# Performance work log

Measured on AMD Instinct MI355X. Metric: run time of the kernel, lower is better.

Reference implementation:

```python
import jax, jax.numpy as jnp
import numpy as np

B, L, H, N = 8, 8192, 128, 32  # batch, seq_len, d_model, d_state//2 (complex)


def setup_inputs() -> dict:
    key = jax.random.key(0)
    ks = jax.random.split(key, 13)
    x = jax.random.normal(ks[0], (B, L, 2), dtype=jnp.float32)
    enc_w = jax.random.normal(ks[1], (2, H), dtype=jnp.float32) * (1.0 / np.sqrt(2.0))
    enc_b = jax.random.normal(ks[2], (H,), dtype=jnp.float32) * 0.01
    # S4D init: dt log-uniform in [1e-3, 1e-1], A = -0.5 + i*pi*n (S4D-Lin)
    u01 = jax.random.uniform(ks[3], (H,), dtype=jnp.float32)
    log_dt = u01 * (np.log(0.1) - np.log(0.001)) + np.log(0.001)
    log_A_real = jnp.full((H, N), np.log(0.5), dtype=jnp.float32)
    A_imag = jnp.broadcast_to(np.pi * jnp.arange(N, dtype=jnp.float32), (H, N)).copy()
    C_re = jax.random.normal(ks[4], (H, N), dtype=jnp.float32) * (0.5 ** 0.5)
    C_im = jax.random.normal(ks[5], (H, N), dtype=jnp.float32) * (0.5 ** 0.5)
    D = jax.random.normal(ks[6], (H,), dtype=jnp.float32)
    out_w = jax.random.normal(ks[7], (2 * H, H), dtype=jnp.float32) * (1.0 / np.sqrt(H))
    out_b = jax.random.normal(ks[8], (2 * H,), dtype=jnp.float32) * 0.01
    dec_w = jax.random.normal(ks[9], (H, 1), dtype=jnp.float32) * (1.0 / np.sqrt(H))
    dec_b = jax.random.normal(ks[10], (1,), dtype=jnp.float32) * 0.01
    return {"x": x, "enc_w": enc_w, "enc_b": enc_b, "log_dt": log_dt,
            "log_A_real": log_A_real, "A_imag": A_imag, "C_re": C_re,
            "C_im": C_im, "D": D, "out_w": out_w, "out_b": out_b,
            "dec_w": dec_w, "dec_b": dec_b}


def reference(x, enc_w, enc_b, log_dt, log_A_real, A_imag, C_re, C_im, D,
              out_w, out_b, dec_w, dec_b):
    # Encoder (B,L,2) -> (B,L,H), then transpose to channels-first (B,H,L)
    u = jnp.einsum('blc,ch->blh', x, enc_w) + enc_b
    u = jnp.swapaxes(u, -1, -2)  # (B,H,L)
    Lx = u.shape[-1]

    # --- S4D kernel (zero-order-hold discretization, diagonal A) ---
    dt = jnp.exp(log_dt)                      # (H,)
    A = -jnp.exp(log_A_real) + 1j * A_imag    # (H,N) complex
    C = C_re + 1j * C_im                      # (H,N)
    dtA = dt[:, None] * A                     # (H,N)
    K_coef = C * (jnp.exp(dtA) - 1.0) / A     # (H,N)
    # Vandermonde: exp(dtA * l), l = 0..L-1  -> (H,N,L)
    vand = jnp.exp(dtA[:, :, None] * jnp.arange(Lx, dtype=jnp.float32))
    K = 2.0 * jnp.einsum('hn,hnl->hl', K_coef, vand).real  # (H,L)

    # --- causal convolution via FFT (length 2L avoids circular wrap) ---
    n = 2 * Lx
    y = jnp.fft.irfft(jnp.fft.rfft(u, n) * jnp.fft.rfft(K, n), n)[..., :Lx]
    y = y + D[:, None] * u                    # skip connection

    # GELU -> pointwise GLU output projection (Conv1d(H, 2H, 1) + GLU)
    y = jax.nn.gelu(y)
    z = jnp.einsum('bhl,gh->bgl', y, out_w) + out_b[None, :, None]  # (B,2H,L)
    a, g = jnp.split(z, 2, axis=1)
    y = a * jax.nn.sigmoid(g)                 # (B,H,L)

    # Mean-pool over sequence, decode to scalar: (B,1)
    pooled = jnp.mean(y, axis=-1)             # (B,H)
    return pooled @ dec_w + dec_b
```

## Files before the change

### kernel.cpp

```cpp
#include <hip/hip_runtime.h>
#include <math.h>

#define B_ 8
#define L_ 8192
#define H_ 128
#define N_ 32
#define C_ 128
#define T_ 64


typedef _Float16 half8 __attribute__((ext_vector_type(8)));
typedef __attribute__((ext_vector_type(4))) float f32x4;

__device__ __forceinline__ float gelu_tanh(float y) {
    float t = 0.7978845608028654f * fmaf(0.044715f, y * y * y, y);
    float e = __expf(2.f * t);
    float th = 1.f - __fdividef(2.f, e + 1.f);
    return 0.5f * y * (1.f + th);
}
__device__ __forceinline__ unsigned short f2h(float f) {
    _Float16 h = (_Float16)f;
    return *(unsigned short*)&h;
}
__device__ __forceinline__ float h2f(unsigned short u) {
    return (float)(*(const _Float16*)&u);
}
__device__ __forceinline__ unsigned int pk2(float a, float b) {
    return (unsigned)f2h(a) | ((unsigned)f2h(b) << 16);
}

__global__ __launch_bounds__(256) void k_s4d(
    const float* __restrict__ x, const float* __restrict__ enc_w,
    const float* __restrict__ enc_b, const float* __restrict__ log_dt,
    const float* __restrict__ log_A_real, const float* __restrict__ A_imag,
    const float* __restrict__ C_re, const float* __restrict__ C_im,
    const float* __restrict__ Dp, const float* __restrict__ out_w,
    unsigned short* __restrict__ Wh, unsigned short* __restrict__ gy)
{
    const int bh = blockIdx.x;
    const int b = bh >> 7, h = bh & (H_ - 1);
    const int tid = threadIdx.x;
    const int lane = tid & 63, wq = tid >> 6;
    const int mrow = lane & 15, quad = lane >> 4;

    __shared__ unsigned short Ut[C_][72];
    __shared__ __align__(16) char scratch[18432];
    __shared__ float2 wTpow[7][N_];
    __shared__ float2 coefs[N_];
    __shared__ float2 ArAi[N_];
    __shared__ float  Kd[64];
    unsigned short* E16 = (unsigned short*)scratch;
    float2*         Sx  = (float2*)scratch;
    unsigned short* St  = (unsigned short*)scratch;

    const float dt = expf(log_dt[h]);
    const float Dh = Dp[h];

    if (tid < N_) {
        int n = tid;
        float Ar = -expf(log_A_real[h * N_ + n]);
        float Ai = A_imag[h * N_ + n];
        ArAi[n] = make_float2(Ar, Ai);
        float ar = dt * Ar, ai = dt * Ai;
        float er = expf(ar);
        float wr = er * cosf(ai), wi = er * sinf(ai);
        float inv = 1.f / (Ar * Ar + Ai * Ai);
        float numr = wr - 1.f, numi = wi;
        float qr = (numr * Ar + numi * Ai) * inv;
        float qi = (numi * Ar - numr * Ai) * inv;
        coefs[n] = make_float2(C_re[h * N_ + n] * qr - C_im[h * N_ + n] * qi,
                               C_re[h * N_ + n] * qi + C_im[h * N_ + n] * qr);
        float arT = dt * Ar * (float)T_, aiT = dt * Ai * (float)T_;
        float erT = expf(arT);
        float pr = erT * cosf(aiT), pi = erT * sinf(aiT);
#pragma unroll
        for (int k = 0; k < 7; ++k) {
            wTpow[k][n] = make_float2(pr, pi);
            float nr = pr * pr - pi * pi;
            pi = 2.f * pr * pi; pr = nr;
        }
    }

    if (b == 0) {
        int g = 2 * h + (tid >> 7), j = tid & 127;
        Wh[g * 128 + j] = f2h(out_w[g * 128 + j]);
    }

    const float ew0 = enc_w[h], ew1 = enc_w[H_ + h], eb = enc_b[h];
    {
        int c = tid >> 1, j0 = (tid & 1) * 32;
        const float4* xp = (const float4*)((const float2*)x + (size_t)b * L_
                                           + c * 64 + j0);
#pragma unroll
        for (int i = 0; i < 16; ++i) {
            float4 xv = xp[i];
            float u0 = fmaf(xv.x, ew0, fmaf(xv.y, ew1, eb));
            float u1 = fmaf(xv.z, ew0, fmaf(xv.w, ew1, eb));
            *(unsigned int*)&Ut[c][j0 + 2 * i] = pk2(u0, u1);
        }
    }
    __syncthreads();

    {
        int t = tid >> 2, q = tid & 3;
        float s = 0.f;
        float ft = (float)t;
#pragma unroll
        for (int k = 0; k < 8; ++k) {
            int n = q * 8 + k;
            float2 cf = coefs[n]; float2 aa = ArAi[n];
            float er = __expf(dt * aa.x * ft);
            float sn, cs; __sincosf(dt * aa.y * ft, &sn, &cs);
            s = fmaf(cf.x, er * cs, s);
            s = fmaf(-cf.y, er * sn, s);
        }
        ((float*)&Ut[t][64])[q] = s;
    }

    {
        f32x4 acc[8];
#pragma unroll
        for (int nt = 0; nt < 8; ++nt) acc[nt] = (f32x4){0.f, 0.f, 0.f, 0.f};
        const int m = wq * 16 + mrow;
        const float2 aa = ArAi[m & 31];
        const float dAr = dt * aa.x, dAi = dt * aa.y;
        const bool isIm = (m >= 32);
#pragma unroll
        for (int ks = 0; ks < 2; ++ks) {
            int k0 = ks * 32 + quad * 8;
            half8 af;
#pragma unroll
            for (int i = 0; i < 8; ++i) {
                float d = (float)(63 - (k0 + i));
                float er = __expf(dAr * d);
                float sn, cs; __sincosf(dAi * d, &sn, &cs);
                af[i] = (_Float16)(isIm ? er * sn : er * cs);
            }
#pragma unroll
            for (int nt = 0; nt < 8; ++nt) {
                half8 bf = *(const half8*)&Ut[nt * 16 + mrow][k0];
                acc[nt] = __builtin_amdgcn_mfma_f32_16x16x32_f16(
                    af, bf, acc[nt], 0, 0, 0);
            }
        }
        const int m0 = wq * 16 + quad * 4;
#pragma unroll
        for (int nt = 0; nt < 8; ++nt) {
            int cc = nt * 16 + mrow;
            unsigned long long w =
                (unsigned long long)pk2(acc[nt][0], acc[nt][1]) |
                ((unsigned long long)pk2(acc[nt][2], acc[nt][3]) << 32);
            *(unsigned long long*)&E16[cc * 72 + m0] = w;
        }
    }
    __syncthreads();

    if (tid < 64) {
        const float* kp = (const float*)&Ut[tid][64];
        Kd[tid] = 2.f * (kp[0] + kp[1] + kp[2] + kp[3])
                  + ((tid == 0) ? Dh : 0.f);
    }

    float zr[16], zi[16];
    const int cHalf = wq & 1, nHalf = wq >> 1;
    const int n0 = nHalf * 16;
    const int c = cHalf * 64 + lane;
    {
        half8 ha = *(const half8*)(E16 + c * 72 + n0);
        half8 hb = *(const half8*)(E16 + c * 72 + n0 + 8);
        half8 hc = *(const half8*)(E16 + c * 72 + 32 + n0);
        half8 hd = *(const half8*)(E16 + c * 72 + 32 + n0 + 8);
#pragma unroll
        for (int j = 0; j < 8; ++j) {
            zr[j] = (float)ha[j];  zr[8 + j] = (float)hb[j];
            zi[j] = (float)hc[j];  zi[8 + j] = (float)hd[j];
        }
    }
    __syncthreads();
#pragma unroll
    for (int k = 0; k < 6; ++k) {
        int s = 1 << k;
        float mask = (lane >= s) ? 1.f : 0.f;
#pragma unroll
        for (int j = 0; j < 16; ++j) {
            float2 q = wTpow[k][n0 + j];
            float vr = __shfl_up(zr[j], s, 64);
            float vi = __shfl_up(zi[j], s, 64);
            float adr = fmaf(q.x, vr, -(q.y * vi));
            float adi = fmaf(q.x, vi, q.y * vr);
            zr[j] = fmaf(mask, adr, zr[j]);
            zi[j] = fmaf(mask, adi, zi[j]);
        }
    }
    if (cHalf == 0) {
#pragma unroll
        for (int j = 0; j < 16; ++j)
            Sx[(n0 + j) * 64 + lane] = make_float2(zr[j], zi[j]);
    }
    __syncthreads();
    if (cHalf == 1) {
#pragma unroll
        for (int j = 0; j < 16; ++j) {
            float2 q = wTpow[6][n0 + j];
            float2 v = Sx[(n0 + j) * 64 + lane];
            zr[j] = fmaf(q.x, v.x, fmaf(-q.y, v.y, zr[j]));
            zi[j] = fmaf(q.x, v.y, fmaf(q.y, v.x, zi[j]));
        }
    }
    {
        bool l0 = (lane == 0);
#pragma unroll
        for (int j = 0; j < 16; ++j) {
            float2 bv = Sx[(n0 + j) * 64 + 63];
            float br = (cHalf == 1) ? bv.x : 0.f;
            float bi = (cHalf == 1) ? bv.y : 0.f;
            float tr = __shfl_up(zr[j], 1, 64);
            float ti = __shfl_up(zi[j], 1, 64);
            zr[j] = l0 ? br : tr;
            zi[j] = l0 ? bi : ti;
        }
    }
    __syncthreads();
    {
        uint4 w0, w1;
        w0.x = pk2(zr[0], zr[1]);   w0.y = pk2(zr[2], zr[3]);
        w0.z = pk2(zr[4], zr[5]);   w0.w = pk2(zr[6], zr[7]);
        w1.x = pk2(zr[8], zr[9]);   w1.y = pk2(zr[10], zr[11]);
        w1.z = pk2(zr[12], zr[13]); w1.w = pk2(zr[14], zr[15]);
        *(uint4*)&St[c * 72 + n0] = w0;
        *(uint4*)&St[c * 72 + n0 + 8] = w1;
        w0.x = pk2(zi[0], zi[1]);   w0.y = pk2(zi[2], zi[3]);
        w0.z = pk2(zi[4], zi[5]);   w0.w = pk2(zi[6], zi[7]);
        w1.x = pk2(zi[8], zi[9]);   w1.y = pk2(zi[10], zi[11]);
        w1.z = pk2(zi[12], zi[13]); w1.w = pk2(zi[14], zi[15]);
        *(uint4*)&St[c * 72 + 32 + n0] = w0;
        *(uint4*)&St[c * 72 + 32 + n0 + 8] = w1;
    }
    __syncthreads();

    {
        f32x4 acc[8];
#pragma unroll
        for (int nt = 0; nt < 8; ++nt) acc[nt] = (f32x4){0.f, 0.f, 0.f, 0.f};
        const int t = wq * 16 + mrow;
#pragma unroll
        for (int ks = 0; ks < 2; ++ks) {
            int k0 = ks * 32 + quad * 8;
            half8 af;
#pragma unroll
            for (int i = 0; i < 8; ++i) {
                int j = k0 + i;
                af[i] = (_Float16)((t >= j) ? Kd[t - j] : 0.f);
            }
#pragma unroll
            for (int nt = 0; nt < 8; ++nt) {
                half8 bf = *(const half8*)&Ut[nt * 16 + mrow][k0];
                acc[nt] = __builtin_amdgcn_mfma_f32_16x16x32_f16(
                    af, bf, acc[nt], 0, 0, 0);
            }
        }
        half8 afP0, afP1;
        {
            float tp1 = (float)(t + 1);
#pragma unroll
            for (int i = 0; i < 8; ++i) {
                int n = quad * 8 + i;
                float2 cf = coefs[n]; float2 aa = ArAi[n];
                float er = __expf(dt * aa.x * tp1);
                float sn, cs; __sincosf(dt * aa.y * tp1, &sn, &cs);
                float wr = er * cs, wi = er * sn;
                afP0[i] = (_Float16)( 2.f * (cf.x * wr - cf.y * wi));
                afP1[i] = (_Float16)(-2.f * (cf.x * wi + cf.y * wr));
            }
        }
#pragma unroll
        for (int ks = 0; ks < 2; ++ks) {
            int k0 = ks * 32 + quad * 8;
            half8 af = ks ? afP1 : afP0;
#pragma unroll
            for (int nt = 0; nt < 8; ++nt) {
                half8 bf = *(const half8*)&St[(nt * 16 + mrow) * 72 + k0];
                acc[nt] = __builtin_amdgcn_mfma_f32_16x16x32_f16(
                    af, bf, acc[nt], 0, 0, 0);
            }
        }
        unsigned short* gyb = gy + (size_t)bh * L_;
#pragma unroll
        for (int nt = 0; nt < 8; ++nt) {
            int cc = nt * 16 + mrow;
#pragma unroll
            for (int r = 0; r < 4; ++r) {
                int tt = wq * 16 + quad * 4 + r;
                gyb[tt * 128 + cc] = f2h(gelu_tanh(acc[nt][r]));
            }
        }
    }
}

__global__ __launch_bounds__(256) void k_mix(
    const unsigned short* __restrict__ Wh, const unsigned short* __restrict__ gy,
    const float* __restrict__ out_b, const float* __restrict__ dec_w,
    float* __restrict__ part)
{
    __shared__ unsigned short Bt[64 * 128];
    __shared__ float red[4];

    const int blk = blockIdx.x;
    const int b = blk >> 7;
    const int t = (blk >> 1) & 63, ch = blk & 1;
    const int tid = threadIdx.x;
    const int wq = tid >> 6, lane = tid & 63;

    const unsigned short* gsrc = gy + (size_t)(b * H_) * L_ + t * 128 + ch * 64;
#pragma unroll
    for (int it = 0; it < 4; ++it) {
        int idx = it * 256 + tid;
        int h = idx >> 3, v0 = (idx & 7) * 8;
        uint4 q = *(const uint4*)(gsrc + (size_t)h * L_ + v0);
        const int sw = (((h >> 3) ^ (idx & 7)) << 3) | (h & 7);
        Bt[(v0 + 0) * 128 + sw] = (unsigned short)(q.x & 0xFFFF);
        Bt[(v0 + 1) * 128 + sw] = (unsigned short)(q.x >> 16);
        Bt[(v0 + 2) * 128 + sw] = (unsigned short)(q.y & 0xFFFF);
        Bt[(v0 + 3) * 128 + sw] = (unsigned short)(q.y >> 16);
        Bt[(v0 + 4) * 128 + sw] = (unsigned short)(q.z & 0xFFFF);
        Bt[(v0 + 5) * 128 + sw] = (unsigned short)(q.z >> 16);
        Bt[(v0 + 6) * 128 + sw] = (unsigned short)(q.w & 0xFFFF);
        Bt[(v0 + 7) * 128 + sw] = (unsigned short)(q.w >> 16);
    }
    __syncthreads();

    const int ga = wq * 32;
    const int gg = 128 + wq * 32;
    const int mrow = lane & 15;
    const int quad = lane >> 4;
    f32x4 accA[2][4], accG[2][4];
#pragma unroll
    for (int mt = 0; mt < 2; ++mt)
#pragma unroll
        for (int nt = 0; nt < 4; ++nt) {
            accA[mt][nt] = (f32x4){0.f, 0.f, 0.f, 0.f};
            accG[mt][nt] = (f32x4){0.f, 0.f, 0.f, 0.f};
        }

#pragma unroll
    for (int k = 0; k < 4; ++k) {
        const int h0 = k * 32 + quad * 8;
        half8 bfr[4];
#pragma unroll
        for (int nt = 0; nt < 4; ++nt) {
            int v = nt * 16 + mrow;
            bfr[nt] = *(const half8*)&Bt[v * 128 +
                                         (((4 * k + quad) ^ (v >> 3)) << 3)];
        }
#pragma unroll
        for (int mt = 0; mt < 2; ++mt) {
            half8 ah = *(const half8*)(Wh + (ga + mt * 16 + mrow) * 128 + h0);
            half8 ag = *(const half8*)(Wh + (gg + mt * 16 + mrow) * 128 + h0);
#pragma unroll
            for (int nt = 0; nt < 4; ++nt) {
                accA[mt][nt] = __builtin_amdgcn_mfma_f32_16x16x32_f16(
                    ah, bfr[nt], accA[mt][nt], 0, 0, 0);
                accG[mt][nt] = __builtin_amdgcn_mfma_f32_16x16x32_f16(
                    ag, bfr[nt], accG[mt][nt], 0, 0, 0);
            }
        }
    }

    float s = 0.f;
#pragma unroll
    for (int mt = 0; mt < 2; ++mt) {
        float4 obA = *(const float4*)(out_b + ga + mt * 16 + quad * 4);
        float4 obG = *(const float4*)(out_b + gg + mt * 16 + quad * 4);
        float4 dv  = *(const float4*)(dec_w + ga + mt * 16 + quad * 4);
#pragma unroll
        for (int nt = 0; nt < 4; ++nt) {
#pragma unroll
            for (int r = 0; r < 4; ++r) {
                float a  = accA[mt][nt][r] + ((const float*)&obA)[r];
                float zg = accG[mt][nt][r] + ((const float*)&obG)[r];
                float sig = __fdividef(1.f, 1.f + __expf(-zg));
                s = fmaf(((const float*)&dv)[r], a * sig, s);
            }
        }
    }
#pragma unroll
    for (int off = 32; off; off >>= 1) s += __shfl_down(s, off, 64);
    if (lane == 0) red[wq] = s;
    __syncthreads();
    if (tid == 0) part[blk] = red[0] + red[1] + red[2] + red[3];
}

__global__ __launch_bounds__(512) void k_final(
    const float* __restrict__ part, const float* __restrict__ dec_b,
    float* __restrict__ out)
{
    int tid = threadIdx.x;
    int b = tid >> 6, lane = tid & 63;
    float s = part[b * 128 + lane] + part[b * 128 + 64 + lane];
#pragma unroll
    for (int off = 32; off; off >>= 1) s += __shfl_down(s, off, 64);
    if (lane == 0) out[b] = fmaf(s, 1.0f / (float)L_, dec_b[0]);
}

extern "C" void kernel_launch(void* const* d_in, const int* in_sizes, int n_in,
                              void* d_out, int out_size, void* d_ws, size_t ws_size,
                              hipStream_t stream)
{
    const float* x         = (const float*)d_in[0];
    const float* enc_w     = (const float*)d_in[1];
    const float* enc_b     = (const float*)d_in[2];
    const float* log_dt    = (const float*)d_in[3];
    const float* log_A_real= (const float*)d_in[4];
    const float* A_imag    = (const float*)d_in[5];
    const float* C_re      = (const float*)d_in[6];
    const float* C_im      = (const float*)d_in[7];
    const float* Dp        = (const float*)d_in[8];
    const float* out_w     = (const float*)d_in[9];
    const float* out_b     = (const float*)d_in[10];
    const float* dec_w     = (const float*)d_in[11];
    const float* dec_b     = (const float*)d_in[12];
    float* out = (float*)d_out;

    char* ws = (char*)d_ws;
    unsigned short* Wh = (unsigned short*)(ws);
    unsigned short* gy = (unsigned short*)(ws + 3211264);
    float* part        = (float*)(ws + 19988480);

    k_s4d<<<B_ * H_, 256, 0, stream>>>(x, enc_w, enc_b, log_dt, log_A_real,
                                       A_imag, C_re, C_im, Dp, out_w, Wh, gy);
    k_mix<<<B_ * 128, 256, 0, stream>>>(Wh, gy, out_b, dec_w, part);
    k_final<<<1, 512, 0, stream>>>(part, dec_b, out);
}
```

Before: 129.9 us.

## Recur Vandermonde powers, skip decayed scan steps, transpose MFMA for packed stores

```diff
diff --git a/kernel.cpp b/kernel.cpp
--- a/kernel.cpp
+++ b/kernel.cpp
@@ -49,6 +49,7 @@
     __shared__ float2 coefs[N_];
     __shared__ float2 ArAi[N_];
     __shared__ float  Kd[64];
+    __shared__ float  sArmax;
     unsigned short* E16 = (unsigned short*)scratch;
     float2*         Sx  = (float2*)scratch;
     unsigned short* St  = (unsigned short*)scratch;
@@ -61,6 +62,11 @@
         float Ar = -expf(log_A_real[h * N_ + n]);
         float Ai = A_imag[h * N_ + n];
         ArAi[n] = make_float2(Ar, Ai);
+        float armx = Ar;
+#pragma unroll
+        for (int off = 16; off; off >>= 1)
+            armx = fmaxf(armx, __shfl_xor(armx, off, 64));
+        if (n == 0) sArmax = armx;
         float ar = dt * Ar, ai = dt * Ai;
         float er = expf(ar);
         float wr = er * cosf(ai), wi = er * sinf(ai);
@@ -125,16 +131,22 @@
         const float2 aa = ArAi[m & 31];
         const float dAr = dt * aa.x, dAi = dt * aa.y;
         const bool isIm = (m >= 32);
+        float s1, c1; __sincosf(dAi, &s1, &c1);
+        const float e1 = __expf(-dAr);
+        const float ir = e1 * c1, ii = -e1 * s1;
 #pragma unroll
         for (int ks = 0; ks < 2; ++ks) {
             int k0 = ks * 32 + quad * 8;
+            float d0 = (float)(63 - k0);
+            float er = __expf(dAr * d0);
+            float sn, cs; __sincosf(dAi * d0, &sn, &cs);
+            float pr = er * cs, pi = er * sn;
             half8 af;
 #pragma unroll
             for (int i = 0; i < 8; ++i) {
-                float d = (float)(63 - (k0 + i));
-                float er = __expf(dAr * d);
-                float sn, cs; __sincosf(dAi * d, &sn, &cs);
-                af[i] = (_Float16)(isIm ? er * sn : er * cs);
+                af[i] = (_Float16)(isIm ? pi : pr);
+                float npr = pr * ir - pi * ii;
+                pi = pr * ii + pi * ir; pr = npr;
             }
 #pragma unroll
             for (int nt = 0; nt < 8; ++nt) {
@@ -177,8 +189,11 @@
         }
     }
     __syncthreads();
+    float mag = __expf(dt * sArmax * 64.f);
 #pragma unroll
     for (int k = 0; k < 6; ++k) {
+        if (mag < 4e-6f) break;
+        mag *= mag;
         int s = 1 << k;
         float mask = (lane >= s) ? 1.f : 0.f;
 #pragma unroll
@@ -198,7 +213,7 @@
             Sx[(n0 + j) * 64 + lane] = make_float2(zr[j], zi[j]);
     }
     __syncthreads();
-    if (cHalf == 1) {
+    if (cHalf == 1 && mag >= 4e-6f) {
 #pragma unroll
         for (int j = 0; j < 16; ++j) {
             float2 q = wTpow[6][n0 + j];
@@ -243,22 +258,6 @@
 #pragma unroll
         for (int nt = 0; nt < 8; ++nt) acc[nt] = (f32x4){0.f, 0.f, 0.f, 0.f};
         const int t = wq * 16 + mrow;
-#pragma unroll
-        for (int ks = 0; ks < 2; ++ks) {
-            int k0 = ks * 32 + quad * 8;
-            half8 af;
-#pragma unroll
-            for (int i = 0; i < 8; ++i) {
-                int j = k0 + i;
-                af[i] = (_Float16)((t >= j) ? Kd[t - j] : 0.f);
-            }
-#pragma unroll
-            for (int nt = 0; nt < 8; ++nt) {
-                half8 bf = *(const half8*)&Ut[nt * 16 + mrow][k0];
-                acc[nt] = __builtin_amdgcn_mfma_f32_16x16x32_f16(
-                    af, bf, acc[nt], 0, 0, 0);
-            }
-        }
         half8 afP0, afP1;
         {
             float tp1 = (float)(t + 1);
@@ -276,23 +275,41 @@
 #pragma unroll
         for (int ks = 0; ks < 2; ++ks) {
             int k0 = ks * 32 + quad * 8;
+            half8 af;
+#pragma unroll
+            for (int i = 0; i < 8; ++i) {
+                int j = k0 + i;
+                af[i] = (_Float16)((t >= j) ? Kd[t - j] : 0.f);
+            }
+#pragma unroll
+            for (int nt = 0; nt < 8; ++nt) {
+                half8 bf = *(const half8*)&Ut[nt * 16 + mrow][k0];
+                acc[nt] = __builtin_amdgcn_mfma_f32_16x16x32_f16(
+                    bf, af, acc[nt], 0, 0, 0);
+            }
+        }
+#pragma unroll
+        for (int ks = 0; ks < 2; ++ks) {
+            int k0 = ks * 32 + quad * 8;
             half8 af = ks ? afP1 : afP0;
 #pragma unroll
             for (int nt = 0; nt < 8; ++nt) {
                 half8 bf = *(const half8*)&St[(nt * 16 + mrow) * 72 + k0];
                 acc[nt] = __builtin_amdgcn_mfma_f32_16x16x32_f16(
-                    af, bf, acc[nt], 0, 0, 0);
-            }
-        }
-        unsigned short* gyb = gy + (size_t)bh * L_;
+                    bf, af, acc[nt], 0, 0, 0);
+            }
+        }
+        unsigned short* gyr = gy + (size_t)bh * L_ + (size_t)t * 128;
 #pragma unroll
         for (int nt = 0; nt < 8; ++nt) {
-            int cc = nt * 16 + mrow;
-#pragma unroll
-            for (int r = 0; r < 4; ++r) {
-                int tt = wq * 16 + quad * 4 + r;
-                gyb[tt * 128 + cc] = f2h(gelu_tanh(acc[nt][r]));
-            }
+            float g0 = gelu_tanh(acc[nt][0]);
+            float g1 = gelu_tanh(acc[nt][1]);
+            float g2 = gelu_tanh(acc[nt][2]);
+            float g3 = gelu_tanh(acc[nt][3]);
+            unsigned long long w =
+                (unsigned long long)pk2(g0, g1) |
+                ((unsigned long long)pk2(g2, g3) << 32);
+            *(unsigned long long*)&gyr[nt * 16 + quad * 4] = w;
         }
     }
 }
```

Measured after the change: 131.5 us. About the same (+1.2%).
